# Performance work log

Measured on AMD Instinct MI355X. Metric: run time of the kernel, lower is better.

Reference implementation:

```python
import jax, jax.numpy as jnp
import numpy as np

NEG_SLOPE = 0.2  # PyG GATConv default


def gat_conv(x, W, a_src, a_dst, b, src, dst, n):
    """Single-head PyG-style GATConv with self-loops already appended to (src, dst)."""
    h = x @ W                                   # [N, F]
    alpha_src = h @ a_src                       # [N]
    alpha_dst = h @ a_dst                       # [N]
    e = alpha_src[src] + alpha_dst[dst]         # [E] per-edge logit (message j->i)
    e = jax.nn.leaky_relu(e, NEG_SLOPE)
    # numerically stable softmax over edges grouped by destination node
    m = jax.ops.segment_max(e, dst, num_segments=n)
    ex = jnp.exp(e - m[dst])
    denom = jax.ops.segment_sum(ex, dst, num_segments=n)
    alpha = ex / denom[dst]                     # [E]
    out = jax.ops.segment_sum(alpha[:, None] * h[src], dst, num_segments=n)
    return out + b


def setup_inputs() -> dict:
    key = jax.random.key(0)
    ks = jax.random.split(key, 16)
    N, C, E = 50000, 128, 800000
    x = jax.random.normal(ks[0], (N, C), dtype=jnp.float32)
    edge_index = jax.random.randint(ks[1], (2, E), 0, N, dtype=jnp.int64)

    def lin(k, din, dout):
        return jax.random.normal(k, (din, dout), dtype=jnp.float32) / np.sqrt(din)

    def att(k, d):
        return jax.random.normal(k, (d,), dtype=jnp.float32) / np.sqrt(d)

    d1, d2, d3 = 2 * C, C // 2, 1
    return {
        "x": x, "edge_index": edge_index,
        "W1": lin(ks[2], C, d1), "as1": att(ks[3], d1), "ad1": att(ks[4], d1), "b1": jnp.zeros((d1,), jnp.float32),
        "W2": lin(ks[5], d1, d2), "as2": att(ks[6], d2), "ad2": att(ks[7], d2), "b2": jnp.zeros((d2,), jnp.float32),
        "W3": lin(ks[8], d2, d3), "as3": att(ks[9], d3), "ad3": att(ks[10], d3), "b3": jnp.zeros((d3,), jnp.float32),
    }


def reference(x, edge_index, W1, as1, ad1, b1, W2, as2, ad2, b2, W3, as3, ad3, b3):
    n = x.shape[0]
    self_loops = jnp.arange(n, dtype=edge_index.dtype)
    src = jnp.concatenate([edge_index[0], self_loops])
    dst = jnp.concatenate([edge_index[1], self_loops])
    # dropout is identity in eval mode
    h = gat_conv(x, W1, as1, ad1, b1, src, dst, n)
    h = jax.nn.elu(h)
    h = gat_conv(h, W2, as2, ad2, b2, src, dst, n)
    h = jax.nn.elu(h)
    return gat_conv(h, W3, as3, ad3, b3, src, dst, n)
```

## Files before the change

kernel.cpp:

```cpp
#include <hip/hip_runtime.h>
#include <hip/hip_bf16.h>
#include <hip/hip_fp16.h>
#include <math.h>

#define NEG_SLOPE 0.2f

typedef __attribute__((ext_vector_type(8))) short      s16x8_t;
typedef __attribute__((ext_vector_type(8))) _Float16   f16x8_t;
typedef __attribute__((ext_vector_type(4))) float      f32x4_t;

struct __align__(8) half4_t { __half2 a, b; };

__global__ __launch_bounds__(256) void prep0_k(
    int* __restrict__ cursor, float* __restrict__ alpha4, int n,
    const float* __restrict__ x, __half* __restrict__ xf, long xcnt8,
    const float* __restrict__ W1, __half* __restrict__ w1t, int K1, int N1,
    const float* __restrict__ W2, __half* __restrict__ w2t, int K2, int N2)
{
    const int gid = blockIdx.x * 256 + threadIdx.x;
    const int gsz = gridDim.x * 256;

    for (int i = gid; i < n; i += gsz) cursor[i] = 0;
    for (long i = gid; i < 4L * n; i += gsz) alpha4[i] = 0.f;
    for (long i = gid; i < xcnt8; i += gsz) {
        const float* src = x + i * 8;
        float4 a = *(const float4*)src;
        float4 b = *(const float4*)(src + 4);
        half4_t o0, o1;
        o0.a = __floats2half2_rn(a.x, a.y);
        o0.b = __floats2half2_rn(a.z, a.w);
        o1.a = __floats2half2_rn(b.x, b.y);
        o1.b = __floats2half2_rn(b.z, b.w);
        *(half4_t*)(xf + i * 8)     = o0;
        *(half4_t*)(xf + i * 8 + 4) = o1;
    }
    for (int i = gid; i < K1 * N1; i += gsz) {
        int k = i / N1, c = i - k * N1;
        w1t[(size_t)c * K1 + k] = __float2half(W1[i]);
    }
    for (int i = gid; i < K2 * N2; i += gsz) {
        int k = i / N2, c = i - k * N2;
        w2t[(size_t)c * K2 + k] = __float2half(W2[i]);
    }
}

__global__ void hist_k(const int* __restrict__ ei, int E, int n, int* __restrict__ deg) {
    int e = blockIdx.x * 256 + threadIdx.x;
    int ET = E + n;
    if (e >= ET) return;
    int d = (e < E) ? ei[E + e] : (e - E);
    atomicAdd(&deg[d], 1);
}

__global__ void scan1_k(const int* __restrict__ deg, int* __restrict__ incl,
                        int* __restrict__ bsums, int n) {
    __shared__ int s[256];
    int tid = threadIdx.x;
    int i = blockIdx.x * 256 + tid;
    int v = (i < n) ? deg[i] : 0;
    s[tid] = v;
    __syncthreads();
    for (int off = 1; off < 256; off <<= 1) {
        int t = (tid >= off) ? s[tid - off] : 0;
        __syncthreads();
        s[tid] += t;
        __syncthreads();
    }
    if (i < n) incl[i] = s[tid];
    if (tid == 255) bsums[blockIdx.x] = s[255];
}

__global__ void scan2_k(int* __restrict__ bsums, int nch) {
    __shared__ int s[256];
    int tid = threadIdx.x;
    int v = (tid < nch) ? bsums[tid] : 0;
    int orig = v;
    s[tid] = v;
    __syncthreads();
    for (int off = 1; off < 256; off <<= 1) {
        int t = (tid >= off) ? s[tid - off] : 0;
        __syncthreads();
        s[tid] += t;
        __syncthreads();
    }
    if (tid < nch) bsums[tid] = s[tid] - orig;
}

__global__ void scan3_k(int* __restrict__ offsets, int* __restrict__ cursor,
                        const int* __restrict__ bsums, int n, int total) {
    int i = blockIdx.x * 256 + threadIdx.x;
    if (i < n) {
        int excl = offsets[i] - cursor[i] + bsums[i >> 8];
        offsets[i] = excl;
        cursor[i]  = excl;
    }
    if (i == 0 && blockIdx.x == 0) offsets[n] = total;
}

__global__ void fill_k(const int* __restrict__ ei, int E, int n,
                       int* __restrict__ cursor, int* __restrict__ csr) {
    int e = blockIdx.x * 256 + threadIdx.x;
    int ET = E + n;
    if (e >= ET) return;
    int s, d;
    if (e < E) { s = ei[e]; d = ei[E + e]; }
    else       { s = e - E; d = e - E; }
    int pos = atomicAdd(&cursor[d], 1);
    csr[pos] = s;
}

__device__ __forceinline__ void gemm_core(const ushort* __restrict__ A,
                                          const ushort* __restrict__ BT,
                                          __half* __restrict__ Ch,
                                          float* __restrict__ asb,
                                          float* __restrict__ adb,
                                          const float* __restrict__ a_src,
                                          const float* __restrict__ a_dst,
                                          int M, int K, int Nc) {
    __shared__ __align__(16) ushort sA[128][40];
    __shared__ __align__(16) ushort sB[64][40];

    const int tid  = threadIdx.x;
    const int lane = tid & 63;
    const int wv   = tid >> 6;
    const int wm   = wv & 1, wn = wv >> 1;
    const int m0   = blockIdx.x << 7;
    const int n0   = blockIdx.y << 6;

    f32x4_t acc[4][2];
#pragma unroll
    for (int i = 0; i < 4; i++)
#pragma unroll
        for (int j = 0; j < 2; j++) acc[i][j] = (f32x4_t){0.f, 0.f, 0.f, 0.f};

    const int arow = tid >> 1;
    const int acb  = (tid & 1) << 4;
    const int brow = tid >> 2;
    const int bkb  = (tid & 3) << 3;

    const s16x8_t zv = {};

    for (int k0 = 0; k0 < K; k0 += 32) {
        {
            const int gr = m0 + arow;
            s16x8_t v0 = zv, v1 = zv;
            if (gr < M) {
                const ushort* pa = A + (size_t)gr * K + k0 + acb;
                v0 = *(const s16x8_t*)pa;
                v1 = *(const s16x8_t*)(pa + 8);
            }
            *(s16x8_t*)&sA[arow][acb]     = v0;
            *(s16x8_t*)&sA[arow][acb + 8] = v1;
        }
        {
            const ushort* pb = BT + (size_t)(n0 + brow) * K + k0 + bkb;
            *(s16x8_t*)&sB[brow][bkb] = *(const s16x8_t*)pb;
        }
        __syncthreads();
        f16x8_t af[4], bf[2];
        const int rbase = (wm << 6) + (lane & 15);
        const int slot  = (lane >> 4) << 3;
#pragma unroll
        for (int mi = 0; mi < 4; mi++)
            af[mi] = *(const f16x8_t*)&sA[rbase + (mi << 4)][slot];
        const int cbase = (wn << 5) + (lane & 15);
#pragma unroll
        for (int ni = 0; ni < 2; ni++)
            bf[ni] = *(const f16x8_t*)&sB[cbase + (ni << 4)][slot];
#pragma unroll
        for (int mi = 0; mi < 4; mi++)
#pragma unroll
            for (int ni = 0; ni < 2; ni++)
                acc[mi][ni] = __builtin_amdgcn_mfma_f32_16x16x32_f16(af[mi], bf[ni], acc[mi][ni], 0, 0, 0);
        __syncthreads();
    }

    const int col0 = n0 + (wn << 5) + (lane & 15);
    const float asv0 = a_src[col0],      adv0 = a_dst[col0];
    const float asv1 = a_src[col0 + 16], adv1 = a_dst[col0 + 16];

#pragma unroll
    for (int mi = 0; mi < 4; mi++) {
        const int row0 = m0 + (wm << 6) + (mi << 4) + ((lane >> 4) << 2);
#pragma unroll
        for (int ni = 0; ni < 2; ni++) {
            const int col = col0 + (ni << 4);
#pragma unroll
            for (int r = 0; r < 4; r++)
                if (row0 + r < M)
                    Ch[(size_t)(row0 + r) * Nc + col] = __float2half(acc[mi][ni][r]);
        }
        float ss[4], sd[4];
#pragma unroll
        for (int r = 0; r < 4; r++) {
            ss[r] = acc[mi][0][r] * asv0 + acc[mi][1][r] * asv1;
            sd[r] = acc[mi][0][r] * adv0 + acc[mi][1][r] * adv1;
        }
#pragma unroll
        for (int off = 1; off < 16; off <<= 1) {
#pragma unroll
            for (int r = 0; r < 4; r++) {
                ss[r] += __shfl_xor(ss[r], off);
                sd[r] += __shfl_xor(sd[r], off);
            }
        }
        if ((lane & 15) == 0) {
#pragma unroll
            for (int r = 0; r < 4; r++)
                if (row0 + r < M) {
                    atomicAdd(&asb[row0 + r], ss[r]);
                    atomicAdd(&adb[row0 + r], sd[r]);
                }
        }
    }
}

__global__ __launch_bounds__(256) void gemm1_k(const ushort* A, const ushort* BT,
                                               __half* Ch, float* asb, float* adb,
                                               const float* a_src, const float* a_dst,
                                               int M, int K, int Nc) {
    gemm_core(A, BT, Ch, asb, adb, a_src, a_dst, M, K, Nc);
}
__global__ __launch_bounds__(256) void gemm2_k(const ushort* A, const ushort* BT,
                                               __half* Ch, float* asb, float* adb,
                                               const float* a_src, const float* a_dst,
                                               int M, int K, int Nc) {
    gemm_core(A, BT, Ch, asb, adb, a_src, a_dst, M, K, Nc);
}

#define DEG_CAP 128

template <int D, bool DO_ELU, bool OUT16, bool L3F>
__device__ __forceinline__ void agg_core(const int* __restrict__ offs,
                                         const int* __restrict__ csr,
                                         const float* __restrict__ asb,
                                         const float* __restrict__ adb,
                                         const __half* __restrict__ h,
                                         const float* __restrict__ bias,
                                         float* __restrict__ out,
                                         __half* __restrict__ o16,
                                         const float* __restrict__ W3,
                                         const float* __restrict__ as3,
                                         const float* __restrict__ ad3,
                                         float* __restrict__ h3o,
                                         float* __restrict__ as3b,
                                         float* __restrict__ ad3b, int n) {
    __shared__ float wsh[4][DEG_CAP];
    __shared__ int   osh[4][DEG_CAP];
    const int wv   = threadIdx.x >> 6;
    const int lane = threadIdx.x & 63;
    const int wid  = (blockIdx.x << 2) + wv;
    const bool active = wid < n;

    int beg = 0, deg = 0;
    float adi = 0.f;
    if (active) {
        beg = offs[wid];
        deg = offs[wid + 1] - beg;
        adi = adb[wid];
    }
    const int degc = deg < DEG_CAP ? deg : DEG_CAP;

    float inv = 0.f;
    if (active) {
        float ssum = 0.f;
        for (int e = lane; e < degc; e += 64) {
            int j = csr[beg + e];
            float v = asb[j] + adi;
            v = v > 0.f ? v : NEG_SLOPE * v;
            v = fminf(fmaxf(v, -60.f), 60.f);
            float w = __expf(v);
            osh[wv][e] = j * (int)(D * sizeof(__half));
            wsh[wv][e] = w;
            ssum += w;
        }
        for (int e = DEG_CAP + lane; e < deg; e += 64) {
            float v = asb[csr[beg + e]] + adi;
            v = v > 0.f ? v : NEG_SLOPE * v;
            v = fminf(fmaxf(v, -60.f), 60.f);
            ssum += __expf(v);
        }
#pragma unroll
        for (int o = 32; o; o >>= 1) ssum += __shfl_xor(ssum, o);
        inv = 1.f / ssum;
    }

    __syncthreads();

    if (!active) return;

    constexpr int U = D / 64;
    float a0[U] = {}, a1[U] = {}, a2[U] = {}, a3[U] = {};
    const char* hb = (const char*)h + (U == 4 ? (lane << 3) : (lane << 1));

    int e = 0;
    for (; e + 4 <= degc; e += 4) {
        int o0 = osh[wv][e], o1 = osh[wv][e + 1], o2 = osh[wv][e + 2], o3 = osh[wv][e + 3];
        float w0 = wsh[wv][e], w1 = wsh[wv][e + 1], w2 = wsh[wv][e + 2], w3 = wsh[wv][e + 3];
        if constexpr (U == 4) {
            const half4_t h0 = *(const half4_t*)(hb + o0);
            const half4_t h1 = *(const half4_t*)(hb + o1);
            const half4_t h2 = *(const half4_t*)(hb + o2);
            const half4_t h3 = *(const half4_t*)(hb + o3);
            float2 f0a = __half22float2(h0.a), f0b = __half22float2(h0.b);
            float2 f1a = __half22float2(h1.a), f1b = __half22float2(h1.b);
            float2 f2a = __half22float2(h2.a), f2b = __half22float2(h2.b);
            float2 f3a = __half22float2(h3.a), f3b = __half22float2(h3.b);
            a0[0] = fmaf(w0, f0a.x, a0[0]); a0[1] = fmaf(w0, f0a.y, a0[1]);
            a0[2] = fmaf(w0, f0b.x, a0[2]); a0[3] = fmaf(w0, f0b.y, a0[3]);
            a1[0] = fmaf(w1, f1a.x, a1[0]); a1[1] = fmaf(w1, f1a.y, a1[1]);
            a1[2] = fmaf(w1, f1b.x, a1[2]); a1[3] = fmaf(w1, f1b.y, a1[3]);
            a2[0] = fmaf(w2, f2a.x, a2[0]); a2[1] = fmaf(w2, f2a.y, a2[1]);
            a2[2] = fmaf(w2, f2b.x, a2[2]); a2[3] = fmaf(w2, f2b.y, a2[3]);
            a3[0] = fmaf(w3, f3a.x, a3[0]); a3[1] = fmaf(w3, f3a.y, a3[1]);
            a3[2] = fmaf(w3, f3b.x, a3[2]); a3[3] = fmaf(w3, f3b.y, a3[3]);
        } else {
            a0[0] = fmaf(w0, __half2float(*(const __half*)(hb + o0)), a0[0]);
            a1[0] = fmaf(w1, __half2float(*(const __half*)(hb + o1)), a1[0]);
            a2[0] = fmaf(w2, __half2float(*(const __half*)(hb + o2)), a2[0]);
            a3[0] = fmaf(w3, __half2float(*(const __half*)(hb + o3)), a3[0]);
        }
    }
    for (; e < degc; ++e) {
        int o0 = osh[wv][e];
        float ww = wsh[wv][e];
        if constexpr (U == 4) {
            const half4_t hv = *(const half4_t*)(hb + o0);
            float2 fa = __half22float2(hv.a), fb = __half22float2(hv.b);
            a0[0] = fmaf(ww, fa.x, a0[0]); a0[1] = fmaf(ww, fa.y, a0[1]);
            a0[2] = fmaf(ww, fb.x, a0[2]); a0[3] = fmaf(ww, fb.y, a0[3]);
        } else {
            a0[0] = fmaf(ww, __half2float(*(const __half*)(hb + o0)), a0[0]);
        }
    }
    for (int eo = DEG_CAP; eo < deg; ++eo) {
        int j = csr[beg + eo];
        float v = asb[j] + adi;
        v = v > 0.f ? v : NEG_SLOPE * v;
        v = fminf(fmaxf(v, -60.f), 60.f);
        float ww = __expf(v);
        int o0 = j * (int)(D * sizeof(__half));
        if constexpr (U == 4) {
            const half4_t hv = *(const half4_t*)(hb + o0);
            float2 fa = __half22float2(hv.a), fb = __half22float2(hv.b);
            a0[0] = fmaf(ww, fa.x, a0[0]); a0[1] = fmaf(ww, fa.y, a0[1]);
            a0[2] = fmaf(ww, fb.x, a0[2]); a0[3] = fmaf(ww, fb.y, a0[3]);
        } else {
            a0[0] = fmaf(ww, __half2float(*(const __half*)(hb + o0)), a0[0]);
        }
    }

    if constexpr (U == 4) {
        float t[4];
#pragma unroll
        for (int u = 0; u < 4; u++) {
            float v = (a0[u] + a1[u] + a2[u] + a3[u]) * inv + bias[(lane << 2) + u];
            if (DO_ELU) v = v > 0.f ? v : expm1f(v);
            t[u] = v;
        }
        if constexpr (OUT16) {
            half4_t o;
            o.a = __floats2half2_rn(t[0], t[1]);
            o.b = __floats2half2_rn(t[2], t[3]);
            *(half4_t*)(o16 + (size_t)wid * D + (lane << 2)) = o;
        } else {
            *(float4*)(out + (size_t)wid * D + (lane << 2)) = make_float4(t[0], t[1], t[2], t[3]);
        }
    } else {
        float t = (a0[0] + a1[0] + a2[0] + a3[0]) * inv + bias[lane];
        if (DO_ELU) t = t > 0.f ? t : expm1f(t);
        if constexpr (L3F) {
            float c = t * W3[lane];
#pragma unroll
            for (int o = 32; o; o >>= 1) c += __shfl_xor(c, o);
            if (lane == 0) {
                h3o[wid]  = c;
                as3b[wid] = c * as3[0];
                ad3b[wid] = c * ad3[0];
            }
        } else {
            out[(size_t)wid * D + lane] = t;
        }
    }
}

__global__ __launch_bounds__(256) void agg1_k(const int* offs, const int* csr,
                                              const float* asb, const float* adb,
                                              const __half* h, const float* bias,
                                              __half* o16, int n) {
    agg_core<256, true, true, false>(offs, csr, asb, adb, h, bias,
                                     nullptr, o16,
                                     nullptr, nullptr, nullptr,
                                     nullptr, nullptr, nullptr, n);
}

__global__ __launch_bounds__(256) void agg2_k(const int* offs, const int* csr,
                                              const float* asb, const float* adb,
                                              const __half* h, const float* bias,
                                              const float* W3, const float* as3,
                                              const float* ad3, float* h3o,
                                              float* as3b, float* ad3b, int n) {
    agg_core<64, true, false, true>(offs, csr, asb, adb, h, bias,
                                    nullptr, nullptr,
                                    W3, as3, ad3, h3o, as3b, ad3b, n);
}

__global__ void agg3_k(const int* __restrict__ offs, const int* __restrict__ csr,
                       const float* __restrict__ asb, const float* __restrict__ adb,
                       const float* __restrict__ h3, const float* __restrict__ b3,
                       float* __restrict__ out, int n) {
    int wid = (blockIdx.x << 2) + (threadIdx.x >> 6);
    int lane = threadIdx.x & 63;
    if (wid >= n) return;
    int beg = offs[wid], end = offs[wid + 1];
    float adi = adb[wid];

    float ssum = 0.f, acc = 0.f;
    for (int e = beg + lane; e < end; e += 64) {
        int j = csr[e];
        float v = asb[j] + adi;
        v = v > 0.f ? v : NEG_SLOPE * v;
        v = fminf(fmaxf(v, -60.f), 60.f);
        float w = __expf(v);
        ssum += w;
        acc = fmaf(w, h3[j], acc);
    }
#pragma unroll
    for (int o = 32; o; o >>= 1) {
        ssum += __shfl_xor(ssum, o);
        acc  += __shfl_xor(acc, o);
    }
    if (lane == 0) out[wid] = acc / ssum + b3[0];
}

extern "C" void kernel_launch(void* const* d_in, const int* in_sizes, int n_in,
                              void* d_out, int out_size, void* d_ws, size_t ws_size,
                              hipStream_t stream) {
    const float* x   = (const float*)d_in[0];
    const int*   ei  = (const int*)d_in[1];
    const float* W1  = (const float*)d_in[2];
    const float* as1 = (const float*)d_in[3];
    const float* ad1 = (const float*)d_in[4];
    const float* b1  = (const float*)d_in[5];
    const float* W2  = (const float*)d_in[6];
    const float* as2 = (const float*)d_in[7];
    const float* ad2 = (const float*)d_in[8];
    const float* b2  = (const float*)d_in[9];
    const float* W3  = (const float*)d_in[10];
    const float* as3 = (const float*)d_in[11];
    const float* ad3 = (const float*)d_in[12];
    const float* b3  = (const float*)d_in[13];

    const int d1 = in_sizes[3];
    const int C  = in_sizes[2] / d1;
    const int N  = in_sizes[0] / C;
    const int E  = in_sizes[1] / 2;
    const int d2 = in_sizes[7];
    const int ET = E + N;

    char* p = (char*)d_ws;
    auto alloc = [&](size_t bytes) -> void* {
        void* q = (void*)p;
        p += (bytes + 255) & ~(size_t)255;
        return q;
    };
    int*    offsets = (int*)alloc(sizeof(int) * (size_t)(N + 1));
    int*    cursor  = (int*)alloc(sizeof(int) * (size_t)N);
    int*    bsums   = (int*)alloc(sizeof(int) * 256);
    int*    csr     = (int*)alloc(sizeof(int) * (size_t)ET);
    float*  alpha   = (float*)alloc(sizeof(float) * (size_t)4 * N);
    float*  as1b = alpha, *ad1b = alpha + N, *as2b = alpha + 2 * N, *ad2b = alpha + 3 * N;
    __half* xf      = (__half*)alloc(sizeof(__half) * (size_t)N * C);
    __half* w1t     = (__half*)alloc(sizeof(__half) * (size_t)C * d1);
    __half* w2t     = (__half*)alloc(sizeof(__half) * (size_t)d1 * d2);
    __half* ch1     = (__half*)alloc(sizeof(__half) * (size_t)N * d1);
    __half* o1      = (__half*)alloc(sizeof(__half) * (size_t)N * d1);
    __half* ch2     = (__half*)alloc(sizeof(__half) * (size_t)N * d2);
    float*  h3      = (float*)alloc(sizeof(float) * (size_t)N);
    float*  as3b    = (float*)alloc(sizeof(float) * (size_t)N);
    float*  ad3b    = (float*)alloc(sizeof(float) * (size_t)N);

    const int eb  = (ET + 255) / 256;
    const int nch = (N + 255) / 256;
    const int wb  = (N + 3) / 4;

    {
        long t8 = (long)N * C / 8;
        prep0_k<<<2048, 256, 0, stream>>>(cursor, alpha, N,
                                          x, xf, t8,
                                          W1, w1t, C, d1,
                                          W2, w2t, d1, d2);
    }

    hist_k<<<eb, 256, 0, stream>>>(ei, E, N, cursor);
    scan1_k<<<nch, 256, 0, stream>>>(cursor, offsets, bsums, N);
    scan2_k<<<1, 256, 0, stream>>>(bsums, nch);
    scan3_k<<<nch, 256, 0, stream>>>(offsets, cursor, bsums, N, ET);
    fill_k<<<eb, 256, 0, stream>>>(ei, E, N, cursor, csr);

    {
        dim3 g((N + 127) / 128, d1 / 64);
        gemm1_k<<<g, 256, 0, stream>>>((const ushort*)xf, (const ushort*)w1t,
                                       ch1, as1b, ad1b, as1, ad1, N, C, d1);
        agg1_k<<<wb, 256, 0, stream>>>(offsets, csr, as1b, ad1b, ch1, b1, o1, N);
    }
    {
        dim3 g((N + 127) / 128, d2 / 64);
        gemm2_k<<<g, 256, 0, stream>>>((const ushort*)o1, (const ushort*)w2t,
                                       ch2, as2b, ad2b, as2, ad2, N, d1, d2);
        agg2_k<<<wb, 256, 0, stream>>>(offsets, csr, as2b, ad2b, ch2, b2,
                                       W3, as3, ad3, h3, as3b, ad3b, N);
    }
    agg3_k<<<wb, 256, 0, stream>>>(offsets, csr, as3b, ad3b, h3, b3, (float*)d_out, N);
}
```

Before: 341.0 us.

## Aggregate layer-1 before GEMM and fold attention vectors into weights

Layer 1 now aggregates the 128-wide input features over neighbours before multiplying by W1, using associativity of the linear map. This halves the gathered row width, since 128 halves are gathered instead of 256. Attention logits are computed from precomputed W·a vectors: layer 1's in prep0, and layer 2's in the GEMM1 epilogue, which also applies bias and ELU to produce o1 directly. GEMM2 drops its alpha epilogue. Each prep0 block recomputes the W1·a reduction serially, and expm1f is added in the GEMM epilogue.

New measurement: 456.5 us. 33.9% more time.

```diff
diff --git a/kernel.cpp b/kernel.cpp
--- a/kernel.cpp
+++ b/kernel.cpp
@@ -1,9 +1,9 @@
 #include <hip/hip_runtime.h>
-#include <hip/hip_bf16.h>
 #include <hip/hip_fp16.h>
 #include <math.h>
 
 #define NEG_SLOPE 0.2f
+#define DEG_CAP 128
 
 typedef __attribute__((ext_vector_type(8))) short      s16x8_t;
 typedef __attribute__((ext_vector_type(8))) _Float16   f16x8_t;
@@ -12,35 +12,48 @@
 struct __align__(8) half4_t { __half2 a, b; };
 
 __global__ __launch_bounds__(256) void prep0_k(
-    int* __restrict__ cursor, float* __restrict__ alpha4, int n,
-    const float* __restrict__ x, __half* __restrict__ xf, long xcnt8,
-    const float* __restrict__ W1, __half* __restrict__ w1t, int K1, int N1,
-    const float* __restrict__ W2, __half* __restrict__ w2t, int K2, int N2)
+    int* __restrict__ cursor, float* __restrict__ zero2n, int n,
+    const float* __restrict__ x, __half* __restrict__ xf,
+    const float* __restrict__ W1, __half* __restrict__ w1t,
+    const float* __restrict__ W2, __half* __restrict__ w2t,
+    const float* __restrict__ as1, const float* __restrict__ ad1,
+    float* __restrict__ asb1, float* __restrict__ adb1,
+    int C, int d1, int d2)
 {
-    const int gid = blockIdx.x * 256 + threadIdx.x;
+    __shared__ float w1s[128], w1d[128];
+    const int tid = threadIdx.x;
+    {
+        int k = tid & 127;
+        const float* av = (tid < 128) ? as1 : ad1;
+        const float* wr = W1 + (size_t)k * d1;
+        float s = 0.f;
+        for (int nn = 0; nn < d1; nn++) s = fmaf(wr[nn], av[nn], s);
+        if (tid < 128) w1s[k] = s; else w1d[k] = s;
+    }
+    __syncthreads();
+
+    const int gid = blockIdx.x * 256 + tid;
     const int gsz = gridDim.x * 256;
 
     for (int i = gid; i < n; i += gsz) cursor[i] = 0;
-    for (long i = gid; i < 4L * n; i += gsz) alpha4[i] = 0.f;
-    for (long i = gid; i < xcnt8; i += gsz) {
-        const float* src = x + i * 8;
-        float4 a = *(const float4*)src;
-        float4 b = *(const float4*)(src + 4);
-        half4_t o0, o1;
-        o0.a = __floats2half2_rn(a.x, a.y);
-        o0.b = __floats2half2_rn(a.z, a.w);
-        o1.a = __floats2half2_rn(b.x, b.y);
-        o1.b = __floats2half2_rn(b.z, b.w);
-        *(half4_t*)(xf + i * 8)     = o0;
-        *(half4_t*)(xf + i * 8 + 4) = o1;
-    }
-    for (int i = gid; i < K1 * N1; i += gsz) {
-        int k = i / N1, c = i - k * N1;
-        w1t[(size_t)c * K1 + k] = __float2half(W1[i]);
-    }
-    for (int i = gid; i < K2 * N2; i += gsz) {
-        int k = i / N2, c = i - k * N2;
-        w2t[(size_t)c * K2 + k] = __float2half(W2[i]);
+    for (int i = gid; i < 2 * n; i += gsz) zero2n[i] = 0.f;
+    for (int i = gid; i < C * d1; i += gsz) {
+        int k = i / d1, c = i - k * d1;
+        w1t[(size_t)c * C + k] = __float2half(W1[i]);
+    }
+    for (int i = gid; i < d1 * d2; i += gsz) {
+        int k = i / d2, c = i - k * d2;
+        w2t[(size_t)c * d1 + k] = __float2half(W2[i]);
+    }
+    const int wvid = gid >> 6, lane = gid & 63, nw = gsz >> 6;
+    for (int row = wvid; row < n; row += nw) {
+        float2 v = *(const float2*)(x + (size_t)row * C + (lane << 1));
+        *(__half2*)(xf + (size_t)row * C + (lane << 1)) = __floats2half2_rn(v.x, v.y);
+        float s = v.x * w1s[lane << 1] + v.y * w1s[(lane << 1) + 1];
+        float d = v.x * w1d[lane << 1] + v.y * w1d[(lane << 1) + 1];
+#pragma unroll
+        for (int o = 32; o; o >>= 1) { s += __shfl_xor(s, o); d += __shfl_xor(d, o); }
+        if (lane == 0) { asb1[row] = s; adb1[row] = d; }
     }
 }
 
@@ -109,16 +122,100 @@
     csr[pos] = s;
 }
 
+__global__ __launch_bounds__(256) void agg1x_k(
+    const int* __restrict__ offs, const int* __restrict__ csr,
+    const float* __restrict__ asb, const float* __restrict__ adb,
+    const __half* __restrict__ xf, __half* __restrict__ z, int n)
+{
+    __shared__ float wsh[4][DEG_CAP];
+    __shared__ int   osh[4][DEG_CAP];
+    const int wv = threadIdx.x >> 6, lane = threadIdx.x & 63;
+    const int wid = (blockIdx.x << 2) + wv;
+    const bool active = wid < n;
+
+    int beg = 0, deg = 0;
+    float adi = 0.f;
+    if (active) { beg = offs[wid]; deg = offs[wid + 1] - beg; adi = adb[wid]; }
+    const int degc = deg < DEG_CAP ? deg : DEG_CAP;
+
+    float inv = 0.f;
+    if (active) {
+        float ssum = 0.f;
+        for (int e = lane; e < degc; e += 64) {
+            int j = csr[beg + e];
+            float v = asb[j] + adi;
+            v = v > 0.f ? v : NEG_SLOPE * v;
+            v = fminf(fmaxf(v, -60.f), 60.f);
+            float w = __expf(v);
+            osh[wv][e] = j << 8;
+            wsh[wv][e] = w;
+            ssum += w;
+        }
+        for (int e = DEG_CAP + lane; e < deg; e += 64) {
+            float v = asb[csr[beg + e]] + adi;
+            v = v > 0.f ? v : NEG_SLOPE * v;
+            v = fminf(fmaxf(v, -60.f), 60.f);
+            ssum += __expf(v);
+        }
+#pragma unroll
+        for (int o = 32; o; o >>= 1) ssum += __shfl_xor(ssum, o);
+        inv = 1.f / ssum;
+    }
+
+    __syncthreads();
+    if (!active) return;
+
+    float c0 = 0.f, d0 = 0.f, c1 = 0.f, d1a = 0.f, c2 = 0.f, d2a = 0.f, c3 = 0.f, d3a = 0.f;
+    const char* hb = (const char*)xf + (lane << 2);
+
+    int e = 0;
+    for (; e + 4 <= degc; e += 4) {
+        int o0 = osh[wv][e], o1 = osh[wv][e + 1], o2 = osh[wv][e + 2], o3 = osh[wv][e + 3];
+        float w0 = wsh[wv][e], w1 = wsh[wv][e + 1], w2 = wsh[wv][e + 2], w3 = wsh[wv][e + 3];
+        float2 f0 = __half22float2(*(const __half2*)(hb + o0));
+        float2 f1 = __half22float2(*(const __half2*)(hb + o1));
+        float2 f2 = __half22float2(*(const __half2*)(hb + o2));
+        float2 f3 = __half22float2(*(const __half2*)(hb + o3));
+        c0 = fmaf(w0, f0.x, c0); d0 = fmaf(w0, f0.y, d0);
+        c1 = fmaf(w1, f1.x, c1); d1a = fmaf(w1, f1.y, d1a);
+        c2 = fmaf(w2, f2.x, c2); d2a = fmaf(w2, f2.y, d2a);
+        c3 = fmaf(w3, f3.x, c3); d3a = fmaf(w3, f3.y, d3a);
+    }
+    for (; e < degc; ++e) {
+        int o0 = osh[wv][e];
+        float w0 = wsh[wv][e];
+        float2 f0 = __half22float2(*(const __half2*)(hb + o0));
+        c0 = fmaf(w0, f0.x, c0); d0 = fmaf(w0, f0.y, d0);
+    }
+    for (int eo = DEG_CAP; eo < deg; ++eo) {
+        int j = csr[beg + eo];
+        float v = asb[j] + adi;
+        v = v > 0.f ? v : NEG_SLOPE * v;
+        v = fminf(fmaxf(v, -60.f), 60.f);
+        float w0 = __expf(v);
+        float2 f0 = __half22float2(*(const __half2*)(hb + (j << 8)));
+        c0 = fmaf(w0, f0.x, c0); d0 = fmaf(w0, f0.y, d0);
+    }
+
+    float t0 = (c0 + c1 + c2 + c3) * inv;
+    float t1 = (d0 + d1a + d2a + d3a) * inv;
+    *(__half2*)(z + (size_t)wid * 128 + (lane << 1)) = __floats2half2_rn(t0, t1);
+}
+
+template <bool EPI>
 __device__ __forceinline__ void gemm_core(const ushort* __restrict__ A,
                                           const ushort* __restrict__ BT,
                                           __half* __restrict__ Ch,
-                                          float* __restrict__ asb,
-                                          float* __restrict__ adb,
-                                          const float* __restrict__ a_src,
-                                          const float* __restrict__ a_dst,
-                                          int M, int K, int Nc) {
+                                          int M, int K, int Nc,
+                                          const float* __restrict__ bias,
+                                          const float* __restrict__ W2, int d2,
+                                          const float* __restrict__ av_s,
+                                          const float* __restrict__ av_d,
+                                          float* __restrict__ asb_o,
+                                          float* __restrict__ adb_o) {
     __shared__ __align__(16) ushort sA[128][40];
     __shared__ __align__(16) ushort sB[64][40];
+    __shared__ float w2s[64], w2d[64];
 
     const int tid  = threadIdx.x;
     const int lane = tid & 63;
@@ -126,6 +223,15 @@
     const int wm   = wv & 1, wn = wv >> 1;
     const int m0   = blockIdx.x << 7;
     const int n0   = blockIdx.y << 6;
+
+    if (EPI && tid < 128) {
+        int c = n0 + (tid & 63);
+        const float* av = (tid < 64) ? av_s : av_d;
+        const float* wr = W2 + (size_t)c * d2;
+        float s = 0.f;
+        for (int m = 0; m < d2; m++) s = fmaf(wr[m], av[m], s);
+        ((tid < 64) ? w2s : w2d)[tid & 63] = s;
+    }
 
     f32x4_t acc[4][2];
 #pragma unroll
@@ -176,89 +282,86 @@
     }
 
     const int col0 = n0 + (wn << 5) + (lane & 15);
-    const float asv0 = a_src[col0],      adv0 = a_dst[col0];
-    const float asv1 = a_src[col0 + 16], adv1 = a_dst[col0 + 16];
+    float bv0 = 0.f, bv1 = 0.f, ws0 = 0.f, ws1 = 0.f, wd0 = 0.f, wd1 = 0.f;
+    if (EPI) {
+        bv0 = bias[col0]; bv1 = bias[col0 + 16];
+        ws0 = w2s[col0 - n0]; ws1 = w2s[col0 + 16 - n0];
+        wd0 = w2d[col0 - n0]; wd1 = w2d[col0 + 16 - n0];
+    }
 
 #pragma unroll
     for (int mi = 0; mi < 4; mi++) {
         const int row0 = m0 + (wm << 6) + (mi << 4) + ((lane >> 4) << 2);
-#pragma unroll
-        for (int ni = 0; ni < 2; ni++) {
-            const int col = col0 + (ni << 4);
-#pragma unroll
-            for (int r = 0; r < 4; r++)
-                if (row0 + r < M)
-                    Ch[(size_t)(row0 + r) * Nc + col] = __float2half(acc[mi][ni][r]);
-        }
-        float ss[4], sd[4];
+        float e0[4], e1[4];
 #pragma unroll
         for (int r = 0; r < 4; r++) {
-            ss[r] = acc[mi][0][r] * asv0 + acc[mi][1][r] * asv1;
-            sd[r] = acc[mi][0][r] * adv0 + acc[mi][1][r] * adv1;
-        }
-#pragma unroll
-        for (int off = 1; off < 16; off <<= 1) {
+            float v0 = acc[mi][0][r], v1 = acc[mi][1][r];
+            if (EPI) {
+                v0 += bv0; v0 = v0 > 0.f ? v0 : expm1f(v0);
+                v1 += bv1; v1 = v1 > 0.f ? v1 : expm1f(v1);
+            }
+            e0[r] = v0; e1[r] = v1;
+            if (row0 + r < M) {
+                Ch[(size_t)(row0 + r) * Nc + col0]      = __float2half(v0);
+                Ch[(size_t)(row0 + r) * Nc + col0 + 16] = __float2half(v1);
+            }
+        }
+        if (EPI) {
+            float ss[4], sd[4];
 #pragma unroll
             for (int r = 0; r < 4; r++) {
-                ss[r] += __shfl_xor(ss[r], off);
-                sd[r] += __shfl_xor(sd[r], off);
+                ss[r] = e0[r] * ws0 + e1[r] * ws1;
+                sd[r] = e0[r] * wd0 + e1[r] * wd1;
             }
-        }
-        if ((lane & 15) == 0) {
-#pragma unroll
-            for (int r = 0; r < 4; r++)
-                if (row0 + r < M) {
-                    atomicAdd(&asb[row0 + r], ss[r]);
-                    atomicAdd(&adb[row0 + r], sd[r]);
+#pragma unroll
+            for (int off = 1; off < 16; off <<= 1) {
+#pragma unroll
+                for (int r = 0; r < 4; r++) {
+                    ss[r] += __shfl_xor(ss[r], off);
+                    sd[r] += __shfl_xor(sd[r], off);
                 }
+            }
+            if ((lane & 15) == 0) {
+#pragma unroll
+                for (int r = 0; r < 4; r++)
+                    if (row0 + r < M) {
+                        atomicAdd(&asb_o[row0 + r], ss[r]);
+                        atomicAdd(&adb_o[row0 + r], sd[r]);
+                    }
+            }
         }
     }
 }
 
 __global__ __launch_bounds__(256) void gemm1_k(const ushort* A, const ushort* BT,
-                                               __half* Ch, float* asb, float* adb,
-                                               const float* a_src, const float* a_dst,
-                                               int M, int K, int Nc) {
-    gemm_core(A, BT, Ch, asb, adb, a_src, a_dst, M, K, Nc);
+                                               __half* Ch, int M, int K, int Nc,
+                                               const float* bias, const float* W2, int d2,
+                                               const float* av_s, const float* av_d,
+                                               float* asb_o, float* adb_o) {
+    gemm_core<true>(A, BT, Ch, M, K, Nc, bias, W2, d2, av_s, av_d, asb_o, adb_o);
 }
 __global__ __launch_bounds__(256) void gemm2_k(const ushort* A, const ushort* BT,
-                                               __half* Ch, float* asb, float* adb,
-                                               const float* a_src, const float* a_dst,
-                                               int M, int K, int Nc) {
-    gemm_core(A, BT, Ch, asb, adb, a_src, a_dst, M, K, Nc);
-}
-
-#define DEG_CAP 128
-
-template <int D, bool DO_ELU, bool OUT16, bool L3F>
-__device__ __forceinline__ void agg_core(const int* __restrict__ offs,
-                                         const int* __restrict__ csr,
-                                         const float* __restrict__ asb,
-                                         const float* __restrict__ adb,
-                                         const __half* __restrict__ h,
-                                         const float* __restrict__ bias,
-                                         float* __restrict__ out,
-                                         __half* __restrict__ o16,
-                                         const float* __restrict__ W3,
-                                         const float* __restrict__ as3,
-                                         const float* __restrict__ ad3,
-                                         float* __restrict__ h3o,
-                                         float* __restrict__ as3b,
-                                         float* __restrict__ ad3b, int n) {
+                                               __half* Ch, int M, int K, int Nc) {
+    gemm_core<false>(A, BT, Ch, M, K, Nc, nullptr, nullptr, 0, nullptr, nullptr, nullptr, nullptr);
+}
+
+__global__ __launch_bounds__(256) void agg2_k(
+    const int* __restrict__ offs, const int* __restrict__ csr,
+    const float* __restrict__ asb, const float* __restrict__ adb,
+    const __half* __restrict__ h, const float* __restrict__ b2,
+    const float* __restrict__ W3, const float* __restrict__ as3,
+    const float* __restrict__ ad3,
+    float* __restrict__ h3o, float* __restrict__ as3b, float* __restrict__ ad3b, int n)
+{
     __shared__ float wsh[4][DEG_CAP];
     __shared__ int   osh[4][DEG_CAP];
-    const int wv   = threadIdx.x >> 6;
-    const int lane = threadIdx.x & 63;
-    const int wid  = (blockIdx.x << 2) + wv;
+    const int wv = threadIdx.x >> 6, lane = threadIdx.x & 63;
+    const int wid = (blockIdx.x << 2) + wv;
     const bool active = wid < n;
 
     int beg = 0, deg = 0;
     float adi = 0.f;
-    if (active) {
-        beg = offs[wid];
-        deg = offs[wid + 1] - beg;
-        adi = adb[wid];
-    }
+    if (active) { beg = offs[wid]; deg = offs[wid + 1] - beg; adi = adb[wid]; }
     const int degc = deg < DEG_CAP ? deg : DEG_CAP;
 
     float inv = 0.f;
@@ -270,7 +373,7 @@
             v = v > 0.f ? v : NEG_SLOPE * v;
             v = fminf(fmaxf(v, -60.f), 60.f);
             float w = __expf(v);
-            osh[wv][e] = j * (int)(D * sizeof(__half));
+            osh[wv][e] = j << 7;
             wsh[wv][e] = w;
             ssum += w;
         }
@@ -286,123 +389,40 @@
     }
 
     __syncthreads();
-
     if (!active) return;
 
-    constexpr int U = D / 64;
-    float a0[U] = {}, a1[U] = {}, a2[U] = {}, a3[U] = {};
-    const char* hb = (const char*)h + (U == 4 ? (lane << 3) : (lane << 1));
+    float c0 = 0.f, c1 = 0.f, c2 = 0.f, c3 = 0.f;
+    const char* hb = (const char*)h + (lane << 1);
 
     int e = 0;
     for (; e + 4 <= degc; e += 4) {
         int o0 = osh[wv][e], o1 = osh[wv][e + 1], o2 = osh[wv][e + 2], o3 = osh[wv][e + 3];
         float w0 = wsh[wv][e], w1 = wsh[wv][e + 1], w2 = wsh[wv][e + 2], w3 = wsh[wv][e + 3];
-        if constexpr (U == 4) {
-            const half4_t h0 = *(const half4_t*)(hb + o0);
-            const half4_t h1 = *(const half4_t*)(hb + o1);
-            const half4_t h2 = *(const half4_t*)(hb + o2);
-            const half4_t h3 = *(const half4_t*)(hb + o3);
-            float2 f0a = __half22float2(h0.a), f0b = __half22float2(h0.b);
-            float2 f1a = __half22float2(h1.a), f1b = __half22float2(h1.b);
-            float2 f2a = __half22float2(h2.a), f2b = __half22float2(h2.b);
-            float2 f3a = __half22float2(h3.a), f3b = __half22float2(h3.b);
-            a0[0] = fmaf(w0, f0a.x, a0[0]); a0[1] = fmaf(w0, f0a.y, a0[1]);
-            a0[2] = fmaf(w0, f0b.x, a0[2]); a0[3] = fmaf(w0, f0b.y, a0[3]);
-            a1[0] = fmaf(w1, f1a.x, a1[0]); a1[1] = fmaf(w1, f1a.y, a1[1]);
-            a1[2] = fmaf(w1, f1b.x, a1[2]); a1[3] = fmaf(w1, f1b.y, a1[3]);
-            a2[0] = fmaf(w2, f2a.x, a2[0]); a2[1] = fmaf(w2, f2a.y, a2[1]);
-            a2[2] = fmaf(w2, f2b.x, a2[2]); a2[3] = fmaf(w2, f2b.y, a2[3]);
-            a3[0] = fmaf(w3, f3a.x, a3[0]); a3[1] = fmaf(w3, f3a.y, a3[1]);
-            a3[2] = fmaf(w3, f3b.x, a3[2]); a3[3] = fmaf(w3, f3b.y, a3[3]);
-        } else {
-            a0[0] = fmaf(w0, __half2float(*(const __half*)(hb + o0)), a0[0]);
-            a1[0] = fmaf(w1, __half2float(*(const __half*)(hb + o1)), a1[0]);
-            a2[0] = fmaf(w2, __half2float(*(const __half*)(hb + o2)), a2[0]);
-            a3[0] = fmaf(w3, __half2float(*(const __half*)(hb + o3)), a3[0]);
-        }
-    }
-    for (; e < degc; ++e) {
-        int o0 = osh[wv][e];
-        float ww = wsh[wv][e];
-        if constexpr (U == 4) {
-            const half4_t hv = *(const half4_t*)(hb + o0);
-            float2 fa = __half22float2(hv.a), fb = __half22float2(hv.b);
-            a0[0] = fmaf(ww, fa.x, a0[0]); a0[1] = fmaf(ww, fa.y, a0[1]);
-            a0[2] = fmaf(ww, fb.x, a0[2]); a0[3] = fmaf(ww, fb.y, a0[3]);
-        } else {
-            a0[0] = fmaf(ww, __half2float(*(const __half*)(hb + o0)), a0[0]);
-        }
-    }
+        c0 = fmaf(w0, __half2float(*(const __half*)(hb + o0)), c0);
+        c1 = fmaf(w1, __half2float(*(const __half*)(hb + o1)), c1);
+        c2 = fmaf(w2, __half2float(*(const __half*)(hb + o2)), c2);
+        c3 = fmaf(w3, __half2float(*(const __half*)(hb + o3)), c3);
+    }
+    for (; e < degc; ++e)
+        c0 = fmaf(wsh[wv][e], __half2float(*(const __half*)(hb + osh[wv][e])), c0);
     for (int eo = DEG_CAP; eo < deg; ++eo) {
         int j = csr[beg + eo];
         float v = asb[j] + adi;
         v = v > 0.f ? v : NEG_SLOPE * v;
         v = fminf(fmaxf(v, -60.f), 60.f);
-        float ww = __expf(v);
-        int o0 = j * (int)(D * sizeof(__half));
-        if constexpr (U == 4) {
-            const half4_t hv = *(const half4_t*)(hb + o0);
-            float2 fa = __half22float2(hv.a), fb = __half22float2(hv.b);
-            a0[0] = fmaf(ww, fa.x, a0[0]); a0[1] = fmaf(ww, fa.y, a0[1]);
-            a0[2] = fmaf(ww, fb.x, a0[2]); a0[3] = fmaf(ww, fb.y, a0[3]);
-        } else {
-            a0[0] = fmaf(ww, __half2float(*(const __half*)(hb + o0)), a0[0]);
-        }
-    }
-
-    if constexpr (U == 4) {
-        float t[4];
-#pragma unroll
-        for (int u = 0; u < 4; u++) {
-            float v = (a0[u] + a1[u] + a2[u] + a3[u]) * inv + bias[(lane << 2) + u];
-            if (DO_ELU) v = v > 0.f ? v : expm1f(v);
-            t[u] = v;
-        }
-        if constexpr (OUT16) {
-            half4_t o;
-            o.a = __floats2half2_rn(t[0], t[1]);
-            o.b = __floats2half2_rn(t[2], t[3]);
-            *(half4_t*)(o16 + (size_t)wid * D + (lane << 2)) = o;
-        } else {
-            *(float4*)(out + (size_t)wid * D + (lane << 2)) = make_float4(t[0], t[1], t[2], t[3]);
-        }
-    } else {
-        float t = (a0[0] + a1[0] + a2[0] + a3[0]) * inv + bias[lane];
-        if (DO_ELU) t = t > 0.f ? t : expm1f(t);
-        if constexpr (L3F) {
-            float c = t * W3[lane];
-#pragma unroll
-            for (int o = 32; o; o >>= 1) c += __shfl_xor(c, o);
-            if (lane == 0) {
-                h3o[wid]  = c;
-                as3b[wid] = c * as3[0];
-                ad3b[wid] = c * ad3[0];
-            }
-        } else {
-            out[(size_t)wid * D + lane] = t;
-        }
-    }
-}
-
-__global__ __launch_bounds__(256) void agg1_k(const int* offs, const int* csr,
-                                              const float* asb, const float* adb,
-                                              const __half* h, const float* bias,
-                                              __half* o16, int n) {
-    agg_core<256, true, true, false>(offs, csr, asb, adb, h, bias,
-                                     nullptr, o16,
-                                     nullptr, nullptr, nullptr,
-                                     nullptr, nullptr, nullptr, n);
-}
-
-__global__ __launch_bounds__(256) void agg2_k(const int* offs, const int* csr,
-                                              const float* asb, const float* adb,
-                                              const __half* h, const float* bias,
-                                              const float* W3, const float* as3,
-                                              const float* ad3, float* h3o,
-                                              float* as3b, float* ad3b, int n) {
-    agg_core<64, true, false, true>(offs, csr, asb, adb, h, bias,
-                                    nullptr, nullptr,
-                                    W3, as3, ad3, h3o, as3b, ad3b, n);
+        c0 = fmaf(__expf(v), __half2float(*(const __half*)(hb + (j << 7))), c0);
+    }
+
+    float t = (c0 + c1 + c2 + c3) * inv + b2[lane];
+    t = t > 0.f ? t : expm1f(t);
+    float c = t * W3[lane];
+#pragma unroll
+    for (int o = 32; o; o >>= 1) c += __shfl_xor(c, o);
+    if (lane == 0) {
+        h3o[wid]  = c;
+        as3b[wid] = c * as3[0];
+        ad3b[wid] = c * ad3[0];
+    }
 }
 
 __global__ void agg3_k(const int* __restrict__ offs, const int* __restrict__ csr,
@@ -468,12 +488,14 @@
     int*    cursor  = (int*)alloc(sizeof(int) * (size_t)N);
     int*    bsums   = (int*)alloc(sizeof(int) * 256);
     int*    csr     = (int*)alloc(sizeof(int) * (size_t)ET);
-    float*  alpha   = (float*)alloc(sizeof(float) * (size_t)4 * N);
-    float*  as1b = alpha, *ad1b = alpha + N, *as2b = alpha + 2 * N, *ad2b = alpha + 3 * N;
+    float*  asb1    = (float*)alloc(sizeof(float) * (size_t)N);
+    float*  adb1    = (float*)alloc(sizeof(float) * (size_t)N);
+    float*  alpha2  = (float*)alloc(sizeof(float) * (size_t)2 * N);
+    float*  as2b = alpha2, *ad2b = alpha2 + N;
     __half* xf      = (__half*)alloc(sizeof(__half) * (size_t)N * C);
+    __half* zbuf    = (__half*)alloc(sizeof(__half) * (size_t)N * C);
     __half* w1t     = (__half*)alloc(sizeof(__half) * (size_t)C * d1);
     __half* w2t     = (__half*)alloc(sizeof(__half) * (size_t)d1 * d2);
-    __half* ch1     = (__half*)alloc(sizeof(__half) * (size_t)N * d1);
     __half* o1      = (__half*)alloc(sizeof(__half) * (size_t)N * d1);
     __half* ch2     = (__half*)alloc(sizeof(__half) * (size_t)N * d2);
     float*  h3      = (float*)alloc(sizeof(float) * (size_t)N);
@@ -484,13 +506,9 @@
     const int nch = (N + 255) / 256;
     const int wb  = (N + 3) / 4;
 
-    {
-        long t8 = (long)N * C / 8;
-        prep0_k<<<2048, 256, 0, stream>>>(cursor, alpha, N,
-                                          x, xf, t8,
-                                          W1, w1t, C, d1,
-                                          W2, w2t, d1, d2);
-    }
+    prep0_k<<<1024, 256, 0, stream>>>(cursor, alpha2, N,
+                                      x, xf, W1, w1t, W2, w2t,
+                                      as1, ad1, asb1, adb1, C, d1, d2);
 
     hist_k<<<eb, 256, 0, stream>>>(ei, E, N, cursor);
     scan1_k<<<nch, 256, 0, stream>>>(cursor, offsets, bsums, N);
@@ -498,18 +516,18 @@
     scan3_k<<<nch, 256, 0, stream>>>(offsets, cursor, bsums, N, ET);
     fill_k<<<eb, 256, 0, stream>>>(ei, E, N, cursor, csr);
 
+    agg1x_k<<<wb, 256, 0, stream>>>(offsets, csr, asb1, adb1, xf, zbuf, N);
     {
         dim3 g((N + 127) / 128, d1 / 64);
-        gemm1_k<<<g, 256, 0, stream>>>((const ushort*)xf, (const ushort*)w1t,
-                                       ch1, as1b, ad1b, as1, ad1, N, C, d1);
-        agg1_k<<<wb, 256, 0, stream>>>(offsets, csr, as1b, ad1b, ch1, b1, o1, N);
+        gemm1_k<<<g, 256, 0, stream>>>((const ushort*)zbuf, (const ushort*)w1t,
+                                       o1, N, C, d1, b1, W2, d2, as2, ad2, as2b, ad2b);
     }
     {
         dim3 g((N + 127) / 128, d2 / 64);
         gemm2_k<<<g, 256, 0, stream>>>((const ushort*)o1, (const ushort*)w2t,
-                                       ch2, as2b, ad2b, as2, ad2, N, d1, d2);
-        agg2_k<<<wb, 256, 0, stream>>>(offsets, csr, as2b, ad2b, ch2, b2,
-                                       W3, as3, ad3, h3, as3b, ad3b, N);
-    }
+                                       ch2, N, d1, d2);
+    }
+    agg2_k<<<wb, 256, 0, stream>>>(offsets, csr, as2b, ad2b, ch2, b2,
+                                   W3, as3, ad3, h3, as3b, ad3b, N);
     agg3_k<<<wb, 256, 0, stream>>>(offsets, csr, as3b, ad3b, h3, b3, (float*)d_out, N);
 }
```
